# Kernel tuning notes

Measured on AMD Instinct MI355X. Metric: run time of the kernel, lower is better.

## Reference

```python
import jax, jax.numpy as jnp
import numpy as np

NQ = 4          # wires=4 in the PennyLane device
NLAYERS = 4     # num_layers default
AX = 'abcd'     # one einsum letter per qubit axis


def _apply_1q(state, U, w):
    """Apply a 2x2 (or batched (B,2,2)) unitary to qubit axis w of state (B,2,2,2,2)."""
    sub = AX[w]
    out = AX[:w] + 'x' + AX[w + 1:]
    if U.ndim == 3:
        return jnp.einsum(f'zx{sub},z{AX}->z{out}', U, state)
    return jnp.einsum(f'x{sub},z{AX}->z{out}', U, state)


def _apply_cnot(state, c, t):
    """CNOT with control qubit c, target qubit t (static wire indices)."""
    s0 = jax.lax.index_in_dim(state, 0, axis=c + 1, keepdims=True)
    s1 = jax.lax.index_in_dim(state, 1, axis=c + 1, keepdims=True)
    s1 = jnp.flip(s1, axis=t + 1)  # flip target amplitudes where control = 1
    return jnp.concatenate([s0, s1], axis=c + 1)


def _rot(phi, theta, omega):
    """PennyLane Rot gate: RZ(omega) @ RY(theta) @ RZ(phi), as a 2x2 complex matrix."""
    c = jnp.cos(theta * 0.5)
    s = jnp.sin(theta * 0.5)
    em = jnp.exp(-0.5j * (phi + omega))   # e^{-i(phi+omega)/2}, complex64 (weak 1j)
    ed = jnp.exp(0.5j * (phi - omega))    # e^{+i(phi-omega)/2}
    return jnp.stack([
        jnp.stack([em * c, -ed * s]),
        jnp.stack([jnp.conj(ed) * s, jnp.conj(em) * c]),
    ])


def _forward(inputs, q_weights):
    B = inputs.shape[0]
    # |0000> statevector, batched
    state = jnp.zeros((B, 2 ** NQ), jnp.complex64).at[:, 0].set(1.0)
    state = state.reshape((B,) + (2,) * NQ)

    # AngleEmbedding with rotation='Y': RY(x_w) on each wire w (per-sample angles)
    half = inputs * 0.5
    c, s = jnp.cos(half), jnp.sin(half)
    for w in range(NQ):
        U = jnp.stack([jnp.stack([c[:, w], -s[:, w]], axis=-1),
                       jnp.stack([s[:, w], c[:, w]], axis=-1)], axis=-2)
        state = _apply_1q(state, U.astype(jnp.complex64), w)

    # One StronglyEntanglingLayers block per layer of q_weights:
    # per-qubit Rot gates followed by a ring of CNOTs (range r=1 for single-layer calls)
    n_layers = q_weights.shape[0]
    for l in range(n_layers):
        for w in range(NQ):
            state = _apply_1q(state, _rot(q_weights[l, w, 0],
                                          q_weights[l, w, 1],
                                          q_weights[l, w, 2]), w)
        for w in range(NQ):
            state = _apply_cnot(state, w, (w + 1) % NQ)

    # <Z_i> for each wire: marginal prob of bit i, contracted with diag(+1,-1)
    probs = state.real ** 2 + state.imag ** 2  # (B,2,2,2,2)
    z = jnp.array([1.0, -1.0], jnp.float32)
    expvals = []
    for w in range(NQ):
        reduce_axes = tuple(i + 1 for i in range(NQ) if i != w)
        p = probs.sum(axis=reduce_axes)  # (B,2)
        expvals.append(p @ z)
    return jnp.stack(expvals, axis=-1)  # (B,4)


def setup_inputs() -> dict:
    key = jax.random.key(0)
    k1, k2 = jax.random.split(key)
    B = 1048576
    inputs = jax.random.normal(k1, (B, NQ), dtype=jnp.float32)
    # glorot_uniform for shape (4,4,3): limit = sqrt(6/(fan_in+fan_out))
    limit = np.sqrt(6.0 / (NQ * 3 + NQ * 3)).astype(np.float32)
    q_weights = jax.random.uniform(k2, (NLAYERS, NQ, 3), dtype=jnp.float32,
                                   minval=-limit, maxval=limit)
    return {"inputs": inputs, "q_weights": q_weights}


def reference(inputs, q_weights):
    return _forward(inputs, q_weights)
```

## Files before the change

kernel.cpp:

```cpp
#include <hip/hip_runtime.h>
#include <math.h>


__global__ void build_C(const float* __restrict__ qw, float* __restrict__ Cg) {
    __shared__ float g[16][8];
    __shared__ float Ur[16][16];
    __shared__ float Ui[16][16];
    __shared__ float ReE[4][16][16];
    int t = threadIdx.x;

    if (t < 16) {
        float phi = qw[t * 3 + 0], theta = qw[t * 3 + 1], omega = qw[t * 3 + 2];
        float ct = cosf(0.5f * theta), st = sinf(0.5f * theta);
        float ha = 0.5f * (phi + omega), hd = 0.5f * (phi - omega);
        float emr = cosf(ha), emi = -sinf(ha);
        float edr = cosf(hd), edi =  sinf(hd);
        g[t][0] =  emr * ct; g[t][1] =  emi * ct;
        g[t][2] = -edr * st; g[t][3] = -edi * st;
        g[t][4] =  edr * st; g[t][5] = -edi * st;
        g[t][6] =  emr * ct; g[t][7] = -emi * ct;
    }
    __syncthreads();

    if (t < 16) {
        float ar[16], ai[16];
#pragma unroll
        for (int b = 0; b < 16; ++b) { ar[b] = (b == t) ? 1.f : 0.f; ai[b] = 0.f; }
#pragma unroll
        for (int l = 0; l < 4; ++l) {
#pragma unroll
            for (int w = 0; w < 4; ++w) {
                int gi = l * 4 + w;
                float u00r = g[gi][0], u00i = g[gi][1], u01r = g[gi][2], u01i = g[gi][3];
                float u10r = g[gi][4], u10i = g[gi][5], u11r = g[gi][6], u11i = g[gi][7];
                int mask = 8 >> w;
#pragma unroll
                for (int b = 0; b < 16; ++b) {
                    if (b & mask) continue;
                    int b1 = b | mask;
                    float xr = ar[b], xi = ai[b], yr = ar[b1], yi = ai[b1];
                    ar[b]  = u00r * xr - u00i * xi + u01r * yr - u01i * yi;
                    ai[b]  = u00r * xi + u00i * xr + u01r * yi + u01i * yr;
                    ar[b1] = u10r * xr - u10i * xi + u11r * yr - u11i * yi;
                    ai[b1] = u10r * xi + u10i * xr + u11r * yi + u11i * yr;
                }
            }
#pragma unroll
            for (int w = 0; w < 4; ++w) {
                int cm = 8 >> w, tm = 8 >> ((w + 1) & 3);
#pragma unroll
                for (int b = 0; b < 16; ++b) {
                    if ((b & cm) && !(b & tm)) {
                        int b1 = b | tm;
                        float tr = ar[b], ti = ai[b];
                        ar[b] = ar[b1]; ai[b] = ai[b1];
                        ar[b1] = tr;    ai[b1] = ti;
                    }
                }
            }
        }
#pragma unroll
        for (int b = 0; b < 16; ++b) { Ur[b][t] = ar[b]; Ui[b][t] = ai[b]; }
    }
    __syncthreads();

    for (int idx = t; idx < 1024; idx += 256) {
        int w = idx >> 8, i = (idx >> 4) & 15, j = idx & 15;
        float acc = 0.f;
#pragma unroll
        for (int b = 0; b < 16; ++b) {
            float z = ((b >> (3 - w)) & 1) ? -1.f : 1.f;
            acc += z * (Ur[b][i] * Ur[b][j] + Ui[b][i] * Ui[b][j]);
        }
        ReE[w][i][j] = acc;
    }
    __syncthreads();

    for (int idx = t; idx < 324; idx += 256) {
        int w = idx & 3, tt = idx >> 2;
        int t01 = tt / 9, t23 = tt % 9;
        int tq[4] = { t01 / 3, t01 % 3, t23 / 3, t23 % 3 };
        int xmask = 0, zmask = 0;
#pragma unroll
        for (int k = 0; k < 4; ++k) {
            if (tq[k] == 1) xmask |= 8 >> k;
            if (tq[k] == 2) zmask |= 8 >> k;
        }
        float acc = 0.f;
#pragma unroll
        for (int i = 0; i < 16; ++i) {
            float sgn = (__popc(i & zmask) & 1) ? -1.f : 1.f;
            acc += sgn * ReE[w][i][i ^ xmask];
        }
        Cg[idx] = acc * 0.0625f;
    }
}

__global__ __launch_bounds__(256) void qlayer_main(
        const float4* __restrict__ x, const float* __restrict__ Cg,
        float4* __restrict__ out, int B) {
    __shared__ __align__(16) float C[324];
    for (int k = threadIdx.x; k < 324; k += 256) C[k] = Cg[k];
    __syncthreads();

    int i = blockIdx.x * 256 + threadIdx.x;
    if (i >= B) return;
    float4 xv = x[i];
    float s0, c0, s1, c1, s2, c2, s3, c3;
    __sincosf(xv.x, &s0, &c0);
    __sincosf(xv.y, &s1, &c1);
    __sincosf(xv.z, &s2, &c2);
    __sincosf(xv.w, &s3, &c3);
    float m0[3] = {1.f, s0, c0}, m1[3] = {1.f, s1, c1};
    float m2[3] = {1.f, s2, c2}, m3[3] = {1.f, s3, c3};
    float M01[9], M23[9];
#pragma unroll
    for (int a = 0; a < 3; ++a)
#pragma unroll
        for (int b = 0; b < 3; ++b) {
            M01[a * 3 + b] = m0[a] * m1[b];
            M23[a * 3 + b] = m2[a] * m3[b];
        }

    float e0 = 0.f, e1 = 0.f, e2 = 0.f, e3 = 0.f;
#pragma unroll
    for (int t01 = 0; t01 < 9; ++t01) {
        float h0 = 0.f, h1 = 0.f, h2 = 0.f, h3 = 0.f;
#pragma unroll
        for (int t23 = 0; t23 < 9; ++t23) {
            const float4 c4 = *(const float4*)&C[(t01 * 9 + t23) * 4];
            float mv = M23[t23];
            h0 = fmaf(c4.x, mv, h0);
            h1 = fmaf(c4.y, mv, h1);
            h2 = fmaf(c4.z, mv, h2);
            h3 = fmaf(c4.w, mv, h3);
        }
        float mu = M01[t01];
        e0 = fmaf(mu, h0, e0);
        e1 = fmaf(mu, h1, e1);
        e2 = fmaf(mu, h2, e2);
        e3 = fmaf(mu, h3, e3);
    }
    out[i] = make_float4(e0, e1, e2, e3);
}

extern "C" void kernel_launch(void* const* d_in, const int* in_sizes, int n_in,
                              void* d_out, int out_size, void* d_ws, size_t ws_size,
                              hipStream_t stream) {
    const float4* x  = (const float4*)d_in[0];
    const float*  qw = (const float*)d_in[1];
    float* Cg = (float*)d_ws;
    float4* out = (float4*)d_out;
    int B = in_sizes[0] / 4;

    hipLaunchKernelGGL(build_C, dim3(1), dim3(256), 0, stream, qw, Cg);

    int blocks = (B + 255) / 256;
    hipLaunchKernelGGL(qlayer_main, dim3(blocks), dim3(256), 0, stream,
                       x, Cg, out, B);
}
```

Measured before the change: 84.55 us.

## Parallelize unitary build across 256 threads and process two samples per thread

The single-block setup kernel now spreads the 16x16 circuit unitary construction over 256 threads. Each gate update ping-pongs between two shared-memory buffers, and each CNOT ring becomes one precomputed row permutation. The setup's trig also switches to fast __sincosf. The main kernel has each thread handle two samples (i and i+half), which amortizes the shared coefficient loads and exposes more independent FMA chains, at the cost of more registers and half as many blocks. The serial setup kernel was a fixed latency cost ahead of the main launch.

```diff
diff --git a/kernel.cpp b/kernel.cpp
--- a/kernel.cpp
+++ b/kernel.cpp
@@ -2,75 +2,73 @@
 #include <math.h>
 
 
-__global__ void build_C(const float* __restrict__ qw, float* __restrict__ Cg) {
+__global__ __launch_bounds__(256) void build_C(const float* __restrict__ qw,
+                                               float* __restrict__ Cg) {
     __shared__ float g[16][8];
-    __shared__ float Ur[16][16];
-    __shared__ float Ui[16][16];
+    __shared__ float Ar[2][16][16];
+    __shared__ float Ai[2][16][16];
     __shared__ float ReE[4][16][16];
     int t = threadIdx.x;
+    int b   = t >> 4;
+    int col = t & 15;
 
     if (t < 16) {
         float phi = qw[t * 3 + 0], theta = qw[t * 3 + 1], omega = qw[t * 3 + 2];
-        float ct = cosf(0.5f * theta), st = sinf(0.5f * theta);
-        float ha = 0.5f * (phi + omega), hd = 0.5f * (phi - omega);
-        float emr = cosf(ha), emi = -sinf(ha);
-        float edr = cosf(hd), edi =  sinf(hd);
-        g[t][0] =  emr * ct; g[t][1] =  emi * ct;
-        g[t][2] = -edr * st; g[t][3] = -edi * st;
-        g[t][4] =  edr * st; g[t][5] = -edi * st;
-        g[t][6] =  emr * ct; g[t][7] = -emi * ct;
+        float st, ct, sha, cha, shd, chd;
+        __sincosf(0.5f * theta, &st, &ct);
+        __sincosf(0.5f * (phi + omega), &sha, &cha);
+        __sincosf(0.5f * (phi - omega), &shd, &chd);
+        g[t][0] =  cha * ct; g[t][1] = -sha * ct;
+        g[t][2] = -chd * st; g[t][3] = -shd * st;
+        g[t][4] =  chd * st; g[t][5] = -shd * st;
+        g[t][6] =  cha * ct; g[t][7] =  sha * ct;
     }
+    Ar[0][b][col] = (b == col) ? 1.f : 0.f;
+    Ai[0][b][col] = 0.f;
     __syncthreads();
 
-    if (t < 16) {
-        float ar[16], ai[16];
+    int perm = b;
 #pragma unroll
-        for (int b = 0; b < 16; ++b) { ar[b] = (b == t) ? 1.f : 0.f; ai[b] = 0.f; }
+    for (int w = 3; w >= 0; --w) {
+        int cm = 8 >> w, tm = 8 >> ((w + 1) & 3);
+        perm = (perm & cm) ? (perm ^ tm) : perm;
+    }
+
+    int p = 0;
+    for (int l = 0; l < 4; ++l) {
 #pragma unroll
-        for (int l = 0; l < 4; ++l) {
-#pragma unroll
-            for (int w = 0; w < 4; ++w) {
-                int gi = l * 4 + w;
-                float u00r = g[gi][0], u00i = g[gi][1], u01r = g[gi][2], u01i = g[gi][3];
-                float u10r = g[gi][4], u10i = g[gi][5], u11r = g[gi][6], u11i = g[gi][7];
-                int mask = 8 >> w;
-#pragma unroll
-                for (int b = 0; b < 16; ++b) {
-                    if (b & mask) continue;
-                    int b1 = b | mask;
-                    float xr = ar[b], xi = ai[b], yr = ar[b1], yi = ai[b1];
-                    ar[b]  = u00r * xr - u00i * xi + u01r * yr - u01i * yi;
-                    ai[b]  = u00r * xi + u00i * xr + u01r * yi + u01i * yr;
-                    ar[b1] = u10r * xr - u10i * xi + u11r * yr - u11i * yi;
-                    ai[b1] = u10r * xi + u10i * xr + u11r * yi + u11i * yr;
-                }
-            }
-#pragma unroll
-            for (int w = 0; w < 4; ++w) {
-                int cm = 8 >> w, tm = 8 >> ((w + 1) & 3);
-#pragma unroll
-                for (int b = 0; b < 16; ++b) {
-                    if ((b & cm) && !(b & tm)) {
-                        int b1 = b | tm;
-                        float tr = ar[b], ti = ai[b];
-                        ar[b] = ar[b1]; ai[b] = ai[b1];
-                        ar[b1] = tr;    ai[b1] = ti;
-                    }
-                }
-            }
+        for (int w = 0; w < 4; ++w) {
+            int gi = l * 4 + w;
+            int m = 8 >> w;
+            int lo = b & ~m, hi = b | m;
+            bool isHi = (b & m) != 0;
+            float cAr = isHi ? g[gi][4] : g[gi][0];
+            float cAi = isHi ? g[gi][5] : g[gi][1];
+            float cBr = isHi ? g[gi][6] : g[gi][2];
+            float cBi = isHi ? g[gi][7] : g[gi][3];
+            float alor = Ar[p][lo][col], aloi = Ai[p][lo][col];
+            float ahir = Ar[p][hi][col], ahii = Ai[p][hi][col];
+            float nr = cAr * alor - cAi * aloi + cBr * ahir - cBi * ahii;
+            float ni = cAr * aloi + cAi * alor + cBr * ahii + cBi * ahir;
+            Ar[1 - p][b][col] = nr;
+            Ai[1 - p][b][col] = ni;
+            p = 1 - p;
+            __syncthreads();
         }
-#pragma unroll
-        for (int b = 0; b < 16; ++b) { Ur[b][t] = ar[b]; Ui[b][t] = ai[b]; }
+        float nr = Ar[p][perm][col], ni = Ai[p][perm][col];
+        Ar[1 - p][b][col] = nr;
+        Ai[1 - p][b][col] = ni;
+        p = 1 - p;
+        __syncthreads();
     }
-    __syncthreads();
 
     for (int idx = t; idx < 1024; idx += 256) {
         int w = idx >> 8, i = (idx >> 4) & 15, j = idx & 15;
         float acc = 0.f;
 #pragma unroll
-        for (int b = 0; b < 16; ++b) {
-            float z = ((b >> (3 - w)) & 1) ? -1.f : 1.f;
-            acc += z * (Ur[b][i] * Ur[b][j] + Ui[b][i] * Ui[b][j]);
+        for (int bb = 0; bb < 16; ++bb) {
+            float z = ((bb >> (3 - w)) & 1) ? -1.f : 1.f;
+            acc += z * (Ar[p][bb][i] * Ar[p][bb][j] + Ai[p][bb][i] * Ai[p][bb][j]);
         }
         ReE[w][i][j] = acc;
     }
@@ -79,13 +77,9 @@
     for (int idx = t; idx < 324; idx += 256) {
         int w = idx & 3, tt = idx >> 2;
         int t01 = tt / 9, t23 = tt % 9;
-        int tq[4] = { t01 / 3, t01 % 3, t23 / 3, t23 % 3 };
-        int xmask = 0, zmask = 0;
-#pragma unroll
-        for (int k = 0; k < 4; ++k) {
-            if (tq[k] == 1) xmask |= 8 >> k;
-            if (tq[k] == 2) zmask |= 8 >> k;
-        }
+        int d0 = t01 / 3, d1 = t01 % 3, d2 = t23 / 3, d3 = t23 % 3;
+        int xmask = ((d0 == 1) << 3) | ((d1 == 1) << 2) | ((d2 == 1) << 1) | (d3 == 1);
+        int zmask = ((d0 == 2) << 3) | ((d1 == 2) << 2) | ((d2 == 2) << 1) | (d3 == 2);
         float acc = 0.f;
 #pragma unroll
         for (int i = 0; i < 16; ++i) {
@@ -103,45 +97,76 @@
     for (int k = threadIdx.x; k < 324; k += 256) C[k] = Cg[k];
     __syncthreads();
 
+    int half = B >> 1;
     int i = blockIdx.x * 256 + threadIdx.x;
-    if (i >= B) return;
-    float4 xv = x[i];
-    float s0, c0, s1, c1, s2, c2, s3, c3;
-    __sincosf(xv.x, &s0, &c0);
-    __sincosf(xv.y, &s1, &c1);
-    __sincosf(xv.z, &s2, &c2);
-    __sincosf(xv.w, &s3, &c3);
-    float m0[3] = {1.f, s0, c0}, m1[3] = {1.f, s1, c1};
-    float m2[3] = {1.f, s2, c2}, m3[3] = {1.f, s3, c3};
-    float M01[9], M23[9];
+    if (i >= half) {
+        if (i == half && (B & 1)) {
+            float4 xv = x[B - 1];
+            float s0, c0, s1, c1, s2, c2, s3, c3;
+            __sincosf(xv.x, &s0, &c0); __sincosf(xv.y, &s1, &c1);
+            __sincosf(xv.z, &s2, &c2); __sincosf(xv.w, &s3, &c3);
+            float m0[3] = {1.f, s0, c0}, m1[3] = {1.f, s1, c1};
+            float m2[3] = {1.f, s2, c2}, m3[3] = {1.f, s3, c3};
+            float e0 = 0.f, e1 = 0.f, e2 = 0.f, e3 = 0.f;
+            for (int t01 = 0; t01 < 9; ++t01)
+                for (int t23 = 0; t23 < 9; ++t23) {
+                    float mv = m0[t01 / 3] * m1[t01 % 3] * m2[t23 / 3] * m3[t23 % 3];
+                    const float4 c4 = *(const float4*)&C[(t01 * 9 + t23) * 4];
+                    e0 = fmaf(c4.x, mv, e0); e1 = fmaf(c4.y, mv, e1);
+                    e2 = fmaf(c4.z, mv, e2); e3 = fmaf(c4.w, mv, e3);
+                }
+            out[B - 1] = make_float4(e0, e1, e2, e3);
+        }
+        return;
+    }
+
+    float4 xa = x[i];
+    float4 xb = x[i + half];
+    float as0, ac0, as1, ac1, as2, ac2, as3, ac3;
+    float bs0, bc0, bs1, bc1, bs2, bc2, bs3, bc3;
+    __sincosf(xa.x, &as0, &ac0); __sincosf(xa.y, &as1, &ac1);
+    __sincosf(xa.z, &as2, &ac2); __sincosf(xa.w, &as3, &ac3);
+    __sincosf(xb.x, &bs0, &bc0); __sincosf(xb.y, &bs1, &bc1);
+    __sincosf(xb.z, &bs2, &bc2); __sincosf(xb.w, &bs3, &bc3);
+
+    float am0[3] = {1.f, as0, ac0}, am1[3] = {1.f, as1, ac1};
+    float am2[3] = {1.f, as2, ac2}, am3[3] = {1.f, as3, ac3};
+    float bm0[3] = {1.f, bs0, bc0}, bm1[3] = {1.f, bs1, bc1};
+    float bm2[3] = {1.f, bs2, bc2}, bm3[3] = {1.f, bs3, bc3};
+    float aM01[9], aM23[9], bM01[9], bM23[9];
 #pragma unroll
     for (int a = 0; a < 3; ++a)
 #pragma unroll
-        for (int b = 0; b < 3; ++b) {
-            M01[a * 3 + b] = m0[a] * m1[b];
-            M23[a * 3 + b] = m2[a] * m3[b];
+        for (int c = 0; c < 3; ++c) {
+            aM01[a * 3 + c] = am0[a] * am1[c];
+            aM23[a * 3 + c] = am2[a] * am3[c];
+            bM01[a * 3 + c] = bm0[a] * bm1[c];
+            bM23[a * 3 + c] = bm2[a] * bm3[c];
         }
 
-    float e0 = 0.f, e1 = 0.f, e2 = 0.f, e3 = 0.f;
+    float ae0 = 0.f, ae1 = 0.f, ae2 = 0.f, ae3 = 0.f;
+    float be0 = 0.f, be1 = 0.f, be2 = 0.f, be3 = 0.f;
 #pragma unroll
     for (int t01 = 0; t01 < 9; ++t01) {
-        float h0 = 0.f, h1 = 0.f, h2 = 0.f, h3 = 0.f;
+        float ah0 = 0.f, ah1 = 0.f, ah2 = 0.f, ah3 = 0.f;
+        float bh0 = 0.f, bh1 = 0.f, bh2 = 0.f, bh3 = 0.f;
 #pragma unroll
         for (int t23 = 0; t23 < 9; ++t23) {
             const float4 c4 = *(const float4*)&C[(t01 * 9 + t23) * 4];
-            float mv = M23[t23];
-            h0 = fmaf(c4.x, mv, h0);
-            h1 = fmaf(c4.y, mv, h1);
-            h2 = fmaf(c4.z, mv, h2);
-            h3 = fmaf(c4.w, mv, h3);
+            float av = aM23[t23], bv = bM23[t23];
+            ah0 = fmaf(c4.x, av, ah0); bh0 = fmaf(c4.x, bv, bh0);
+            ah1 = fmaf(c4.y, av, ah1); bh1 = fmaf(c4.y, bv, bh1);
+            ah2 = fmaf(c4.z, av, ah2); bh2 = fmaf(c4.z, bv, bh2);
+            ah3 = fmaf(c4.w, av, ah3); bh3 = fmaf(c4.w, bv, bh3);
         }
-        float mu = M01[t01];
-        e0 = fmaf(mu, h0, e0);
-        e1 = fmaf(mu, h1, e1);
-        e2 = fmaf(mu, h2, e2);
-        e3 = fmaf(mu, h3, e3);
+        float au = aM01[t01], bu = bM01[t01];
+        ae0 = fmaf(au, ah0, ae0); be0 = fmaf(bu, bh0, be0);
+        ae1 = fmaf(au, ah1, ae1); be1 = fmaf(bu, bh1, be1);
+        ae2 = fmaf(au, ah2, ae2); be2 = fmaf(bu, bh2, be2);
+        ae3 = fmaf(au, ah3, ae3); be3 = fmaf(bu, bh3, be3);
     }
-    out[i] = make_float4(e0, e1, e2, e3);
+    out[i]        = make_float4(ae0, ae1, ae2, ae3);
+    out[i + half] = make_float4(be0, be1, be2, be3);
 }
 
 extern "C" void kernel_launch(void* const* d_in, const int* in_sizes, int n_in,
@@ -155,7 +180,9 @@
 
     hipLaunchKernelGGL(build_C, dim3(1), dim3(256), 0, stream, qw, Cg);
 
-    int blocks = (B + 255) / 256;
+    int half = B >> 1;
+    int blocks = (half + 255) / 256;
+    if (blocks < 1) blocks = 1;
     hipLaunchKernelGGL(qlayer_main, dim3(blocks), dim3(256), 0, stream,
                        x, Cg, out, B);
 }
```

New measurement: 81.10 us. 4.1% less time.
